# Optimization experiments

Measured on AMD Instinct MI355X. Metric: run time of the kernel, lower is better.

## Reference

```python
import jax, jax.numpy as jnp
import numpy as np


def setup_inputs() -> dict:
    key = jax.random.key(0)
    ks = jax.random.split(key, 8)
    B, C, H, W = 8, 256, 64, 64
    s = 1.0 / np.sqrt(C)
    return {
        "x": jax.random.normal(ks[0], (B, C, H, W), dtype=jnp.float32),
        "wq": jax.random.normal(ks[1], (C, C), dtype=jnp.float32) * s,
        "bq": jax.random.normal(ks[2], (C,), dtype=jnp.float32) * 0.01,
        "wk": jax.random.normal(ks[3], (C, C), dtype=jnp.float32) * s,
        "bk": jax.random.normal(ks[4], (C,), dtype=jnp.float32) * 0.01,
        "wv": jax.random.normal(ks[5], (C, C), dtype=jnp.float32) * s,
        "bv": jax.random.normal(ks[6], (C,), dtype=jnp.float32) * 0.01,
        "gamma": jax.random.normal(ks[7], (1,), dtype=jnp.float32) * 0.1,
    }


def reference(x, wq, bq, wk, bk, wv, bv, gamma):
    B, C, H, W = x.shape
    N = H * W
    xf = x.reshape(B, C, N)  # flatten spatial -> tokens
    # 1x1 convs == per-pixel linear maps over channels
    q = jnp.einsum('oc,bcn->bon', wq, xf) + bq[None, :, None]  # [B,C,N]
    k = jnp.einsum('oc,bcn->bon', wk, xf) + bk[None, :, None]  # [B,C,N]
    v = jnp.einsum('oc,bcn->bon', wv, xf) + bv[None, :, None]  # [B,C,N]
    # energy[b,n,m] = <q[:, n], k[:, m]>  (query tokens x key tokens)
    energy = jnp.einsum('bcn,bcm->bnm', q, k)  # [B,N,N]
    attention = jax.nn.softmax(energy, axis=-1)
    # out = V @ attention^T : out[b,c,n] = sum_m v[b,c,m] * attention[b,n,m]
    out = jnp.einsum('bcm,bnm->bcn', v, attention).reshape(B, C, H, W)
    return gamma[0] * out + x
```

## Files before the change

kernel.cpp:

```cpp
#include <hip/hip_runtime.h>
#include <hip/hip_bf16.h>
#include <cstdint>


typedef short short8 __attribute__((ext_vector_type(8)));
typedef short short4v __attribute__((ext_vector_type(4)));
typedef float f32x4 __attribute__((ext_vector_type(4)));
typedef unsigned int uint4v __attribute__((ext_vector_type(4)));

#define MFMA16(a, b, c) __builtin_amdgcn_mfma_f32_16x16x32_bf16((a), (b), (c), 0, 0, 0)
#define LOG2E 1.4426950408889634f

__device__ __forceinline__ unsigned short f2bf(float f) {
    union { float f; unsigned int u; } v;
    v.f = f;
    unsigned int u = v.u;
    return (unsigned short)((u + 0x7fffu + ((u >> 16) & 1u)) >> 16);
}

__device__ __forceinline__ void load_lds16(const unsigned short* g, unsigned short* l) {
    __builtin_amdgcn_global_load_lds(
        (const __attribute__((address_space(1))) unsigned int*)g,
        (__attribute__((address_space(3))) unsigned int*)l, 16, 0, 0);
}

__device__ __forceinline__ float rowmax16_dpp(float x) {
    int v;
    v = __builtin_amdgcn_update_dpp(0, __float_as_int(x), 0x121, 0xf, 0xf, false);
    x = fmaxf(x, __int_as_float(v));
    v = __builtin_amdgcn_update_dpp(0, __float_as_int(x), 0x122, 0xf, 0xf, false);
    x = fmaxf(x, __int_as_float(v));
    v = __builtin_amdgcn_update_dpp(0, __float_as_int(x), 0x124, 0xf, 0xf, false);
    x = fmaxf(x, __int_as_float(v));
    v = __builtin_amdgcn_update_dpp(0, __float_as_int(x), 0x128, 0xf, 0xf, false);
    x = fmaxf(x, __int_as_float(v));
    return x;
}

__device__ __forceinline__ float wavemax_bcast(float x) {
    int v;
    v = __builtin_amdgcn_update_dpp(__float_as_int(x), __float_as_int(x), 0x142, 0xf, 0xf, false);
    x = fmaxf(x, __int_as_float(v));
    v = __builtin_amdgcn_update_dpp(__float_as_int(x), __float_as_int(x), 0x143, 0xf, 0xf, false);
    x = fmaxf(x, __int_as_float(v));
    return __int_as_float(__builtin_amdgcn_readlane(__float_as_int(x), 63));
}

__global__ __launch_bounds__(256) void wcvt_kernel(
    const float* __restrict__ wq, const float* __restrict__ wk,
    const float* __restrict__ wv, unsigned short* __restrict__ Wb)
{
    int idx = (blockIdx.x * 256 + threadIdx.x) * 4;
    const float* src = (idx < 65536) ? wq : ((idx < 131072) ? wk : wv);
    float4 f = *(const float4*)(src + (idx & 65535));
    short4v s = { (short)f2bf(f.x), (short)f2bf(f.y), (short)f2bf(f.z), (short)f2bf(f.w) };
    *(short4v*)(Wb + idx) = s;
}

__global__ __launch_bounds__(256, 2) void qkv_kernel(
    const float* __restrict__ x, const unsigned short* __restrict__ Wb,
    const float* __restrict__ bq, const float* __restrict__ bk,
    const float* __restrict__ bv,
    unsigned short* __restrict__ Qc, unsigned short* __restrict__ Kr,
    unsigned short* __restrict__ Vc)
{
    const int C = 256, N = 4096;
    __shared__ __align__(16) unsigned short Xt[32][264];

    const int tid  = threadIdx.x;
    const int bid  = blockIdx.x;
    const int b    = bid >> 7;
    const int n0   = (bid & 127) * 32;
    const int wave = tid >> 6;
    const int lane = tid & 63;
    const int quad = lane >> 4;
    const int l16  = lane & 15;
    const int ch0  = wave * 64;

    {
        const int token = tid & 31;
        const int cg    = tid >> 5;
        const float* xb = x + ((size_t)b * C) * N + n0 + token;
#pragma unroll
        for (int p = 0; p < 8; p++) {
            int c0 = p * 32 + cg * 4;
            float f0 = xb[(size_t)(c0 + 0) * N];
            float f1 = xb[(size_t)(c0 + 1) * N];
            float f2 = xb[(size_t)(c0 + 2) * N];
            float f3 = xb[(size_t)(c0 + 3) * N];
            short4v s = { (short)f2bf(f0), (short)f2bf(f1), (short)f2bf(f2), (short)f2bf(f3) };
            *(short4v*)(&Xt[token][c0]) = s;
        }
    }
    __syncthreads();

    f32x4 acc[4][2];

#pragma unroll
    for (int ct = 0; ct < 4; ct++)
#pragma unroll
        for (int tt = 0; tt < 2; tt++) acc[ct][tt] = (f32x4){0.f, 0.f, 0.f, 0.f};
#pragma unroll
    for (int kc = 0; kc < 8; kc++) {
        const int ko = kc * 32 + quad * 8;
        short8 ax0 = *(const short8*)(&Xt[l16][ko]);
        short8 ax1 = *(const short8*)(&Xt[16 + l16][ko]);
#pragma unroll
        for (int ct = 0; ct < 4; ct++) {
            short8 wf = *(const short8*)(Wb + (ch0 + ct * 16 + l16) * 256 + ko);
            acc[ct][0] = MFMA16(ax0, wf, acc[ct][0]);
            acc[ct][1] = MFMA16(ax1, wf, acc[ct][1]);
        }
    }
#pragma unroll
    for (int ct = 0; ct < 4; ct++) {
        const int ch = ch0 + ct * 16 + l16;
        const float biq = bq[ch];
        uint4v qv;
#pragma unroll
        for (int r = 0; r < 4; r++) {
            unsigned int lo = f2bf((acc[ct][0][r] + biq) * LOG2E);
            unsigned int hi = f2bf((acc[ct][1][r] + biq) * LOG2E);
            qv[r] = lo | (hi << 16);
        }
        *(uint4v*)(Qc + ((size_t)b * C + ch) * N + n0 + quad * 8) = qv;
    }

#pragma unroll
    for (int ct = 0; ct < 4; ct++)
#pragma unroll
        for (int tt = 0; tt < 2; tt++) acc[ct][tt] = (f32x4){0.f, 0.f, 0.f, 0.f};
#pragma unroll
    for (int kc = 0; kc < 8; kc++) {
        const int ko = kc * 32 + quad * 8;
        short8 ax0 = *(const short8*)(&Xt[l16][ko]);
        short8 ax1 = *(const short8*)(&Xt[16 + l16][ko]);
#pragma unroll
        for (int ct = 0; ct < 4; ct++) {
            short8 wf = *(const short8*)(Wb + (2 << 16) + (ch0 + ct * 16 + l16) * 256 + ko);
            acc[ct][0] = MFMA16(ax0, wf, acc[ct][0]);
            acc[ct][1] = MFMA16(ax1, wf, acc[ct][1]);
        }
    }
#pragma unroll
    for (int ct = 0; ct < 4; ct++) {
        const int ch = ch0 + ct * 16 + l16;
        const float biv = bv[ch];
        uint4v vv;
#pragma unroll
        for (int r = 0; r < 4; r++) {
            unsigned int lo = f2bf(acc[ct][0][r] + biv);
            unsigned int hi = f2bf(acc[ct][1][r] + biv);
            vv[r] = lo | (hi << 16);
        }
        *(uint4v*)(Vc + ((size_t)b * C + ch) * N + n0 + quad * 8) = vv;
    }

#pragma unroll
    for (int ct = 0; ct < 4; ct++)
#pragma unroll
        for (int tt = 0; tt < 2; tt++) acc[ct][tt] = (f32x4){0.f, 0.f, 0.f, 0.f};
#pragma unroll
    for (int kc = 0; kc < 8; kc++) {
        const int ko = kc * 32 + quad * 8;
        short8 ax0 = *(const short8*)(&Xt[l16][ko]);
        short8 ax1 = *(const short8*)(&Xt[16 + l16][ko]);
#pragma unroll
        for (int ct = 0; ct < 4; ct++) {
            short8 wf = *(const short8*)(Wb + (1 << 16) + (ch0 + ct * 16 + l16) * 256 + ko);
            acc[ct][0] = MFMA16(ax0, wf, acc[ct][0]);
            acc[ct][1] = MFMA16(ax1, wf, acc[ct][1]);
        }
    }
    __syncthreads();
#pragma unroll
    for (int ct = 0; ct < 4; ct++) {
        const int ch = ch0 + ct * 16 + l16;
        const float bik = bk[ch];
#pragma unroll
        for (int tt = 0; tt < 2; tt++) {
#pragma unroll
            for (int r = 0; r < 4; r++)
                Xt[tt * 16 + quad * 4 + r][ch] = f2bf(acc[ct][tt][r] + bik);
        }
    }
    __syncthreads();
#pragma unroll
    for (int p = 0; p < 2; p++) {
        int chunk = p * 256 + tid;
        int tok = chunk >> 4;
        int cc  = (chunk & 15) * 16;
        *(short8*)(Kr + ((size_t)b * N + n0 + tok) * C + cc) = *(const short8*)(&Xt[tok][cc]);
    }
}

__global__ __launch_bounds__(512, 2) void attn_kernel(
    const unsigned short* __restrict__ Qc,
    const unsigned short* __restrict__ Kr,
    const unsigned short* __restrict__ Vc,
    const float* __restrict__ x,
    const float* __restrict__ gamma,
    float* __restrict__ out)
{
    const int C = 256, N = 4096;
    __shared__ __align__(16) unsigned short KV[2][32768];
    __shared__ float Lw[8][32];
    __shared__ float MwL[4];

    const int tid  = threadIdx.x;
    const int wave = tid >> 6;
    const int ks   = wave >> 2;
    const int w4   = wave & 3;
    const int lane = tid & 63;
    const int quad = lane >> 4;
    const int l16  = lane & 15;
    const int bid  = blockIdx.x;
    const int b    = bid & 7;
    const int q0   = (bid >> 3) * 128 + w4 * 32;

    const unsigned short* kb  = Kr + (size_t)b * N * C;
    const unsigned short* vcb = Vc + (size_t)b * C * N;

    short8 aqL[8], aqH[8];
    {
        const unsigned int* qb32 = (const unsigned int*)(Qc + (size_t)b * C * N);
#pragma unroll
        for (int f = 0; f < 8; f++) {
#pragma unroll
            for (int j = 0; j < 8; j++) {
                size_t i32 = ((size_t)(f * 32 + quad * 8 + j) * N + q0) / 2 + l16;
                unsigned int u = qb32[i32];
                aqL[f][j] = (short)(u & 0xffff);
                aqH[f][j] = (short)(u >> 16);
            }
        }
    }

    f32x4 oL[16], oH[16];
#pragma unroll
    for (int t = 0; t < 16; t++) {
        oL[t] = (f32x4){0.f, 0.f, 0.f, 0.f};
        oH[t] = (f32x4){0.f, 0.f, 0.f, 0.f};
    }
    float m_w = -__builtin_inff();
    float l_pL = 0.f, l_pH = 0.f;

    auto stage = [&](int buf, int m0) {
        unsigned short* dst = &KV[buf][0];
#pragma unroll
        for (int p = 0; p < 4; p++) {
            int chunk = p * 512 + tid;
            int half = chunk >> 10;
            int idx  = chunk & 1023;
            int key = idx >> 5;
            int j = (idx & 31) ^ (key & 31);
            load_lds16(kb + (size_t)(half * 2048 + m0 + key) * C + j * 8,
                       dst + half * 16384 + idx * 8);
        }
#pragma unroll
        for (int p = 0; p < 4; p++) {
            int chunk = p * 512 + tid;
            int half = chunk >> 10;
            int idx  = chunk & 1023;
            int c = idx >> 2;
            int s = idx & 3;
            int j = (s - (c >> 1)) & 3;
            load_lds16(vcb + (size_t)c * N + half * 2048 + m0 + j * 8,
                       dst + half * 16384 + 8192 + idx * 8);
        }
    };

    f32x4 tL0, tL1, tH0, tH1;

    auto qk = [&](int buf) {
        const unsigned short* Kb = &KV[buf][ks * 16384];
        f32x4 a0 = {0.f,0.f,0.f,0.f}, a1 = {0.f,0.f,0.f,0.f};
        f32x4 b0 = {0.f,0.f,0.f,0.f}, b1 = {0.f,0.f,0.f,0.f};
#pragma unroll
        for (int f = 0; f < 8; f++) {
            const int j = f * 4 + quad;
            int k0 = l16, k1 = 16 + l16;
            short8 kf0 = *(const short8*)(Kb + (k0 * 32 + (j ^ (k0 & 31))) * 8);
            short8 kf1 = *(const short8*)(Kb + (k1 * 32 + (j ^ (k1 & 31))) * 8);
            a0 = MFMA16(kf0, aqL[f], a0);
            a1 = MFMA16(kf1, aqL[f], a1);
            b0 = MFMA16(kf0, aqH[f], b0);
            b1 = MFMA16(kf1, aqH[f], b1);
        }
        tL0 = a0; tL1 = a1; tH0 = b0; tH1 = b1;
    };

    const int vsl = ((quad + (l16 >> 1)) & 3) * 8;

    stage(0, 0);
    __syncthreads();
    stage(1, 32);
    qk(0);

    for (int it = 0; it < 64; ++it) {
        float mx = fmaxf(fmaxf(fmaxf(tL0[0], tL0[1]), fmaxf(tL0[2], tL0[3])),
                         fmaxf(fmaxf(tL1[0], tL1[1]), fmaxf(tL1[2], tL1[3])));
        mx = fmaxf(mx, fmaxf(fmaxf(fmaxf(tH0[0], tH0[1]), fmaxf(tH0[2], tH0[3])),
                             fmaxf(fmaxf(tH1[0], tH1[1]), fmaxf(tH1[2], tH1[3]))));
        mx = rowmax16_dpp(mx);
        mx = wavemax_bcast(mx);

        if (mx > m_w + 8.0f) {
            const float al = exp2f(m_w - mx);
            m_w = mx;
            l_pL *= al; l_pH *= al;
#pragma unroll
            for (int t = 0; t < 16; t++) { oL[t] *= al; oH[t] *= al; }
        }
        const float mn = m_w;

        uint4v apLu, apHu;
#pragma unroll
        for (int w = 0; w < 4; w++) {
            float e0 = exp2f(tL0[w] - mn);
            float e1 = exp2f(tL1[w] - mn);
            l_pL += e0 + e1;
            union { __hip_bfloat162 v; unsigned int u; } cv;
            cv.v = __float22bfloat162_rn(float2{e0, e1});
            apLu[w] = cv.u;
            float g0 = exp2f(tH0[w] - mn);
            float g1 = exp2f(tH1[w] - mn);
            l_pH += g0 + g1;
            union { __hip_bfloat162 v; unsigned int u; } cw;
            cw.v = __float22bfloat162_rn(float2{g0, g1});
            apHu[w] = cw.u;
        }
        short8 apL, apH;
        {
            union { uint4v u; short8 s; } c1; c1.u = apLu; apL = c1.s;
            union { uint4v u; short8 s; } c2; c2.u = apHu; apH = c2.s;
        }

        if (it < 63) {
            __syncthreads();
            qk((it + 1) & 1);
        }

        {
            const unsigned short* Vb = &KV[it & 1][ks * 16384 + 8192];
#pragma unroll
            for (int t = 0; t < 16; t++) {
                short8 vf = *(const short8*)(Vb + t * 512 + l16 * 32 + vsl);
                oL[t] = MFMA16(apL, vf, oL[t]);
                oH[t] = MFMA16(apH, vf, oH[t]);
            }
        }
        __syncthreads();
        if (it < 62) stage(it & 1, (it + 2) * 32);
    }

    l_pL += __shfl_xor(l_pL, 16);
    l_pL += __shfl_xor(l_pL, 32);
    l_pH += __shfl_xor(l_pH, 16);
    l_pH += __shfl_xor(l_pH, 32);
    if (quad == 0) {
        Lw[wave][l16] = l_pL;
        Lw[wave][16 + l16] = l_pH;
    }

    float* CombF = (float*)(&KV[0][0]);
    __syncthreads();
    if (ks == 1) {
#pragma unroll
        for (int t = 0; t < 16; t++) {
#pragma unroll
            for (int r = 0; r < 4; r++) {
                CombF[(size_t)(w4 * 32 + quad * 4 + r) * 256 + t * 16 + l16] = oL[t][r];
                CombF[(size_t)(w4 * 32 + 16 + quad * 4 + r) * 256 + t * 16 + l16] = oH[t][r];
            }
        }
        if (lane == 0) MwL[w4] = m_w;
    }
    __syncthreads();
    if (ks == 0) {
        const float g = gamma[0];
        const float m2w = MwL[w4];
        const float mt = fmaxf(m_w, m2w);
        const float f1 = exp2f(m_w - mt);
        const float f2 = exp2f(m2w - mt);
        float linv[2][4];
#pragma unroll
        for (int h = 0; h < 2; h++)
#pragma unroll
            for (int r = 0; r < 4; r++) {
                const int q = h * 16 + quad * 4 + r;
                linv[h][r] = g / (Lw[w4][q] * f1 + Lw[4 + w4][q] * f2);
            }
#pragma unroll
        for (int t = 0; t < 16; t++) {
            const int c = t * 16 + l16;
#pragma unroll
            for (int h = 0; h < 2; h++) {
                const int nb = q0 + h * 16 + quad * 4;
                f32x4 o1 = h ? oH[t] : oL[t];
                f32x4 ov;
#pragma unroll
                for (int r = 0; r < 4; r++) {
                    float o2 = CombF[(size_t)(w4 * 32 + h * 16 + quad * 4 + r) * 256 + c];
                    ov[r] = (o1[r] * f1 + o2 * f2) * linv[h][r];
                }
                size_t idx = ((size_t)(b * C + c)) * N + nb;
                f32x4 xv = *(const f32x4*)(x + idx);
                *(f32x4*)(out + idx) = ov + xv;
            }
        }
    }
}

extern "C" void kernel_launch(void* const* d_in, const int* in_sizes, int n_in,
                              void* d_out, int out_size, void* d_ws, size_t ws_size,
                              hipStream_t stream) {
    const int B = 8, C = 256, N = 4096;
    const float* x     = (const float*)d_in[0];
    const float* wq    = (const float*)d_in[1];
    const float* bq    = (const float*)d_in[2];
    const float* wk    = (const float*)d_in[3];
    const float* bk    = (const float*)d_in[4];
    const float* wv    = (const float*)d_in[5];
    const float* bv    = (const float*)d_in[6];
    const float* gamma = (const float*)d_in[7];
    float* out = (float*)d_out;

    unsigned short* Qc = (unsigned short*)d_ws;
    unsigned short* Kr = Qc + (size_t)B * C * N;
    unsigned short* Vc = Kr + (size_t)B * N * C;
    unsigned short* Wb = Vc + (size_t)B * C * N;

    wcvt_kernel<<<dim3(192), 256, 0, stream>>>(wq, wk, wv, Wb);
    qkv_kernel<<<dim3(1024), 256, 0, stream>>>(x, Wb, bq, bk, bv, Qc, Kr, Vc);
    attn_kernel<<<dim3(256), 512, 0, stream>>>(Qc, Kr, Vc, x, gamma, out);
}
```

Before: 362.5 us.

## Stagger wave-group schedules so QK and PV MFMA phases interleave across halves

```diff
diff --git a/kernel.cpp b/kernel.cpp
--- a/kernel.cpp
+++ b/kernel.cpp
@@ -245,28 +245,28 @@
     float m_w = -__builtin_inff();
     float l_pL = 0.f, l_pH = 0.f;
 
-    auto stage = [&](int buf, int m0) {
-        unsigned short* dst = &KV[buf][0];
+    const int gtid = tid & 255;
+    auto stageK = [&](int buf, int m0) {
+        unsigned short* dst = &KV[buf][ks * 16384];
 #pragma unroll
         for (int p = 0; p < 4; p++) {
-            int chunk = p * 512 + tid;
-            int half = chunk >> 10;
-            int idx  = chunk & 1023;
-            int key = idx >> 5;
-            int j = (idx & 31) ^ (key & 31);
-            load_lds16(kb + (size_t)(half * 2048 + m0 + key) * C + j * 8,
-                       dst + half * 16384 + idx * 8);
-        }
+            int chunk = p * 256 + gtid;
+            int key = chunk >> 5;
+            int j = (chunk & 31) ^ (key & 31);
+            load_lds16(kb + (size_t)(ks * 2048 + m0 + key) * C + j * 8,
+                       dst + chunk * 8);
+        }
+    };
+    auto stageV = [&](int buf, int m0) {
+        unsigned short* dst = &KV[buf][ks * 16384 + 8192];
 #pragma unroll
         for (int p = 0; p < 4; p++) {
-            int chunk = p * 512 + tid;
-            int half = chunk >> 10;
-            int idx  = chunk & 1023;
-            int c = idx >> 2;
-            int s = idx & 3;
+            int chunk = p * 256 + gtid;
+            int c = chunk >> 2;
+            int s = chunk & 3;
             int j = (s - (c >> 1)) & 3;
-            load_lds16(vcb + (size_t)c * N + half * 2048 + m0 + j * 8,
-                       dst + half * 16384 + 8192 + idx * 8);
+            load_lds16(vcb + (size_t)c * N + ks * 2048 + m0 + j * 8,
+                       dst + chunk * 8);
         }
     };
 
@@ -276,6 +276,7 @@
         const unsigned short* Kb = &KV[buf][ks * 16384];
         f32x4 a0 = {0.f,0.f,0.f,0.f}, a1 = {0.f,0.f,0.f,0.f};
         f32x4 b0 = {0.f,0.f,0.f,0.f}, b1 = {0.f,0.f,0.f,0.f};
+        __builtin_amdgcn_s_setprio(1);
 #pragma unroll
         for (int f = 0; f < 8; f++) {
             const int j = f * 4 + quad;
@@ -287,17 +288,13 @@
             b0 = MFMA16(kf0, aqH[f], b0);
             b1 = MFMA16(kf1, aqH[f], b1);
         }
+        __builtin_amdgcn_s_setprio(0);
         tL0 = a0; tL1 = a1; tH0 = b0; tH1 = b1;
     };
 
     const int vsl = ((quad + (l16 >> 1)) & 3) * 8;
 
-    stage(0, 0);
-    __syncthreads();
-    stage(1, 32);
-    qk(0);
-
-    for (int it = 0; it < 64; ++it) {
+    auto smpv = [&](int buf) {
         float mx = fmaxf(fmaxf(fmaxf(tL0[0], tL0[1]), fmaxf(tL0[2], tL0[3])),
                          fmaxf(fmaxf(tL1[0], tL1[1]), fmaxf(tL1[2], tL1[3])));
         mx = fmaxf(mx, fmaxf(fmaxf(fmaxf(tH0[0], tH0[1]), fmaxf(tH0[2], tH0[3])),
@@ -336,22 +333,40 @@
             union { uint4v u; short8 s; } c2; c2.u = apHu; apH = c2.s;
         }
 
-        if (it < 63) {
+        const unsigned short* Vb = &KV[buf][ks * 16384 + 8192];
+        __builtin_amdgcn_s_setprio(1);
+#pragma unroll
+        for (int t = 0; t < 16; t++) {
+            short8 vf = *(const short8*)(Vb + t * 512 + l16 * 32 + vsl);
+            oL[t] = MFMA16(apL, vf, oL[t]);
+            oH[t] = MFMA16(apH, vf, oH[t]);
+        }
+        __builtin_amdgcn_s_setprio(0);
+    };
+
+    stageK(0, 0);
+    if (ks == 0) stageV(0, 0);
+    __syncthreads();
+
+    if (ks == 0) {
+        for (int it = 0; it < 64; ++it) {
+            if (it < 63) {
+                stageK((it + 1) & 1, (it + 1) * 32);
+                stageV((it + 1) & 1, (it + 1) * 32);
+            }
+            qk(it & 1);
+            smpv(it & 1);
             __syncthreads();
-            qk((it + 1) & 1);
-        }
-
-        {
-            const unsigned short* Vb = &KV[it & 1][ks * 16384 + 8192];
-#pragma unroll
-            for (int t = 0; t < 16; t++) {
-                short8 vf = *(const short8*)(Vb + t * 512 + l16 * 32 + vsl);
-                oL[t] = MFMA16(apL, vf, oL[t]);
-                oH[t] = MFMA16(apH, vf, oH[t]);
-            }
-        }
-        __syncthreads();
-        if (it < 62) stage(it & 1, (it + 2) * 32);
+        }
+    } else {
+        for (int it = 0; it < 64; ++it) {
+            if (it < 63) stageK((it + 1) & 1, (it + 1) * 32);
+            stageV(it & 1, it * 32);
+            if (it > 0) smpv((it - 1) & 1);
+            qk(it & 1);
+            __syncthreads();
+        }
+        smpv(1);
     }
 
     l_pL += __shfl_xor(l_pL, 16);
```

New measurement: 382.0 us. 1.05x slower.
